# Optimization experiments

Hardware: AMD Instinct MI355X
Metric: run time of the kernel (lower is better)

## Reference

```python
import jax, jax.numpy as jnp
import numpy as np
import math

# ---- static config (matches init_kwargs) ----
MUL = 16                       # multiplicity of 0e and 1o irreps in/out
IN_DIM = 4 * MUL               # 16x0e + 16x1o -> 16 + 48 = 64 channels
DIAMETER = 7.0
RADIUS = DIAMETER / 2.0
NRB = 8                        # num_radial_basis
STEPS = (1.0, 1.0, 1.0)
N_PATHS = 5                    # 0x0->0, 1x1->0, 0x1->1, 1x0->1, 1x1->1
WEIGHT_NUMEL = N_PATHS * MUL * MUL  # 1280


def _lattice():
    axes = []
    for st in STEPS:
        s = math.floor(RADIUS / st)
        axes.append(np.arange(-s, s + 1.0) * st)
    return np.stack(np.meshgrid(*axes, indexing='ij'), axis=-1).astype(np.float32)  # [kx,ky,kz,3]


def _radial_emb(r):
    # e3nn soft_one_hot_linspace, basis='smooth_finite', cutoff=True
    values = np.linspace(0.0, RADIUS, NRB + 2)[1:-1].astype(np.float32)
    step = values[1] - values[0]
    diff = (r[..., None] - values) / step
    def u(t):  # soft unit step: exp(-1/t) for t>0 else 0
        return np.where(t > 0.0, np.exp(-1.0 / np.where(t > 0.0, t, 1.0)), 0.0)
    return (1.14136 * math.e ** 2 * u(diff + 1.0) * u(1.0 - diff)).astype(np.float32)


def _spherical_harmonics(lat):
    # normalize=True, normalization='component': Y0 = 1, Y1 = sqrt(3) * unit_vec
    n = np.linalg.norm(lat, axis=-1, keepdims=True)
    unit = np.where(n > 0, lat / np.where(n > 0, n, 1.0), 0.0)
    return np.ones(lat.shape[:-1], np.float32), (math.sqrt(3.0) * unit).astype(np.float32)


_LAT = _lattice()
_EMB = jnp.asarray(_radial_emb(np.linalg.norm(_LAT, axis=-1)))  # [kx,ky,kz,NRB]
_sh0_np, _sh1_np = _spherical_harmonics(_LAT)
_SH0, _SH1 = jnp.asarray(_sh0_np), jnp.asarray(_sh1_np)
_eps_np = np.zeros((3, 3, 3), np.float32)
for _i, _j, _k in [(0, 1, 2), (1, 2, 0), (2, 0, 1)]:
    _eps_np[_i, _j, _k] = 1.0
    _eps_np[_i, _k, _j] = -1.0
_EPS = jnp.asarray(_eps_np)


def _build_kernel(tp_weight):
    """Radial-basis matmul + CG tensor-product -> conv kernel [out,in,kx,ky,kz]."""
    kx, ky, kz = _LAT.shape[:3]
    nk = kx * ky * kz
    w = jnp.einsum('xyzb,bn->xyzn', _EMB, tp_weight) / nk
    w = w.reshape(kx, ky, kz, N_PATHS, MUL, MUL)
    w1, w2, w3, w4, w5 = [w[..., p, :, :] for p in range(N_PATHS)]
    # e3nn path weights ('component' norm, 'element' path norm): sqrt(dim_out / fan_in)
    a0 = math.sqrt(1.0 / (2 * MUL))  # -> 0e: paths 1,2 each mul1*mul2 = MUL
    a1 = math.sqrt(3.0 / (3 * MUL))  # -> 1o: paths 3,4,5
    c1 = a0                          # w3j(0,0,0) = 1
    c2 = a0 / math.sqrt(3.0)         # w3j(1,1,0) = delta/sqrt(3)
    c3 = a1 / math.sqrt(3.0)         # w3j(0,1,1) = delta/sqrt(3)
    c4 = a1 / math.sqrt(3.0)         # w3j(1,0,1) = delta/sqrt(3)
    c5 = a1 / math.sqrt(6.0)         # w3j(1,1,1) = eps/sqrt(6)
    Kss = c1 * _SH0[..., None, None] * w1                                  # [k,u,o]
    Kvs = c2 * jnp.einsum('xyzi,xyzuo->xyzuio', _SH1, w2)                  # [k,u,3,o]
    Ksv = c3 * jnp.einsum('xyzk,xyzuo->xyzuok', _SH1, w3)                  # [k,u,o,3]
    eye3 = jnp.eye(3, dtype=w.dtype)
    Kvv = (c4 * jnp.einsum('xyz,ik,xyzuo->xyzuiok', _SH0, eye3, w4)
           + c5 * jnp.einsum('ijk,xyzj,xyzuo->xyzuiok', _EPS, _SH1, w5))   # [k,u,3,o,3]
    top = jnp.concatenate([Kss, Ksv.reshape(kx, ky, kz, MUL, 3 * MUL)], axis=-1)
    bot = jnp.concatenate([Kvs.reshape(kx, ky, kz, 3 * MUL, MUL),
                           Kvv.reshape(kx, ky, kz, 3 * MUL, 3 * MUL)], axis=-1)
    K = jnp.concatenate([top, bot], axis=-2)                               # [kx,ky,kz,in,out]
    return jnp.transpose(K, (4, 3, 0, 1, 2))                               # oixyz


def setup_inputs() -> dict:
    key = jax.random.key(0)
    k1, k2, k3, k4 = jax.random.split(key, 4)
    x = jax.random.normal(k1, (2, IN_DIM, 40, 40, 40), jnp.float32)
    sc_w0 = jax.random.normal(k2, (MUL, MUL), jnp.float32)
    sc_w1 = jax.random.normal(k3, (MUL, MUL), jnp.float32)
    tp_weight = jax.random.normal(k4, (NRB, WEIGHT_NUMEL), jnp.float32)
    return {"x": x, "sc_w0": sc_w0, "sc_w1": sc_w1, "tp_weight": tp_weight}


def reference(x, sc_w0, sc_w1, tp_weight):
    B = x.shape[0]
    sp = x.shape[2:]
    inv = 1.0 / math.sqrt(MUL)  # e3nn Linear fan-in normalization
    x0 = x[:, :MUL]                                  # [B,MUL,D,H,W]
    x1 = x[:, MUL:].reshape(B, MUL, 3, *sp)          # [B,MUL,3,D,H,W]
    sc0 = jnp.einsum('uo,budhw->bodhw', sc_w0, x0) * inv
    sc1 = jnp.einsum('uo,buidhw->boidhw', sc_w1, x1) * inv
    sc = jnp.concatenate([sc0, sc1.reshape(B, 3 * MUL, *sp)], axis=1)
    K = _build_kernel(tp_weight)
    pad = [(s // 2, s // 2) for s in K.shape[2:]]
    conv = jax.lax.conv_general_dilated(
        x, K, window_strides=(1, 1, 1), padding=pad,
        dimension_numbers=('NCDHW', 'OIDHW', 'NCDHW'))
    return sc + conv
```

## Files before the change

### kernel.cpp

```cpp
#include <hip/hip_runtime.h>
#include <stdint.h>


#define NT_REAL 179
#define NT_PAD  180
#define NGRP    45

typedef short s16x8 __attribute__((ext_vector_type(8)));
typedef float f32x4 __attribute__((ext_vector_type(4)));

struct Taps {
  int n;
  short dl16[NT_PAD];
  unsigned char dz[NT_PAD], dy[NT_PAD], dx[NT_PAD];
};
constexpr Taps mk_taps() {
  Taps t{};
  t.n = 0;
  for (int a = 0; a < 7; ++a)
    for (int b = 0; b < 7; ++b)
      for (int c = 0; c < 7; ++c) {
        int d2 = (a-3)*(a-3) + (b-3)*(b-3) + (c-3)*(c-3);
        if (d2 <= 12) {
          t.dz[t.n] = (unsigned char)a; t.dy[t.n] = (unsigned char)b;
          t.dx[t.n] = (unsigned char)c;
          t.dl16[t.n] = (short)((a*14 + b)*16 + c);
          ++t.n;
        }
      }
  for (int i = t.n; i < NT_PAD; ++i) {
    t.dz[i] = 3; t.dy[i] = 3; t.dx[i] = 3; t.dl16[i] = t.dl16[0];
  }
  return t;
}
__device__ constexpr Taps TAPS = mk_taps();
static_assert(mk_taps().n == NT_REAL, "tap count");

static __device__ inline unsigned short f2bf(float f) {
  unsigned int u = __float_as_uint(f);
  unsigned int r = u + 0x7FFFu + ((u >> 16) & 1u);
  return (unsigned short)(r >> 16);
}

__device__ __forceinline__ void gl_lds16(const void* g, void* s) {
  __builtin_amdgcn_global_load_lds(
      (const __attribute__((address_space(1))) void*)g,
      (__attribute__((address_space(3))) void*)s, 16, 0, 0);
}

__global__ void build_w(const float* __restrict__ scw0, const float* __restrict__ scw1,
                        const float* __restrict__ tpw, unsigned short* __restrict__ Bwp) {
  int t = blockIdx.x;
  int tid = threadIdx.x;
  __shared__ float wsm[5][16][16];

  int dz = TAPS.dz[t], dy = TAPS.dy[t], dx = TAPS.dx[t];
  float fz = dz - 3.0f, fy = dy - 3.0f, fx = dx - 3.0f;
  float d2 = fz*fz + fy*fy + fx*fx;
  float r = sqrtf(d2);

  const float step = 3.5f / 9.0f;
  const float Cc = 1.14136f * 7.38905609893065f;
  float emb[8];
  for (int bb = 0; bb < 8; ++bb) {
    float diff = (r - step * (bb + 1)) / step;
    float t1 = diff + 1.0f, t2 = 1.0f - diff;
    float u1 = (t1 > 0.0f) ? expf(-1.0f / t1) : 0.0f;
    float u2 = (t2 > 0.0f) ? expf(-1.0f / t2) : 0.0f;
    emb[bb] = Cc * u1 * u2;
  }

  int u = tid >> 4, o = tid & 15;
  for (int p = 0; p < 5; ++p) {
    float acc = 0.0f;
    int nidx = (p * 16 + u) * 16 + o;
    for (int bb = 0; bb < 8; ++bb) acc += emb[bb] * tpw[bb * 1280 + nidx];
    wsm[p][u][o] = acc * (1.0f / 343.0f);
  }
  __syncthreads();

  float invr = (d2 > 0.0f) ? (1.7320508075688772f / r) : 0.0f;
  float sh[3] = { fz * invr, fy * invr, fx * invr };

  bool center = (dz == 3 && dy == 3 && dx == 3);
  bool padt = (t >= NT_REAL);
  const float c1 = 0.17677669529663687f;
  const float c2 = 0.10206207261596575f;
  const float c3 = 0.14433756729740643f;
  const float c4 = 0.14433756729740643f;
  const float c5 = 0.10206207261596575f;
  const float inv = 0.25f;

  for (int e = tid; e < 4096; e += 256) {
    int ich = e & 63, och = e >> 6;
    float v = 0.0f;
    if (!padt) {
      if (och < 16) {
        if (ich < 16) {
          v = c1 * wsm[0][ich][och];
          if (center) v += inv * scw0[ich * 16 + och];
        } else {
          int qq = ich - 16; int uu = qq / 3, ii = qq % 3;
          v = c2 * sh[ii] * wsm[1][uu][och];
        }
      } else {
        int qo = och - 16; int oo = qo / 3, kk = qo % 3;
        if (ich < 16) {
          v = c3 * sh[kk] * wsm[2][ich][oo];
        } else {
          int qi = ich - 16; int uu = qi / 3, ii = qi % 3;
          if (ii == kk) {
            v = c4 * wsm[3][uu][oo];
            if (center) v += inv * scw1[uu * 16 + oo];
          } else {
            int jj = 3 - ii - kk;
            float sgn = (((kk - ii + 3) % 3) == 2) ? 1.0f : -1.0f;
            v = c5 * sgn * sh[jj] * wsm[4][uu][oo];
          }
        }
      }
    }
    int chunk = ich >> 3, j = ich & 7, q = t & 3, grp = t >> 2;
    int nt = och >> 4, n = och & 15;
    size_t idx = (((((size_t)chunk * NGRP + grp) * 4 + nt) * 4 + q) * 16 + n) * 8 + j;
    Bwp[idx] = f2bf(v);
  }
}

__global__ void pad_cvt(const float* __restrict__ x, unsigned short* __restrict__ Xp) {
  __shared__ float buf[46 * 65];
  int blk = blockIdx.x;
  int yp = blk % 46; int t = blk / 46; int zp = t % 46; int b = t / 46;
  int iz = zp - 3, iy = yp - 3;
  bool rowin = ((unsigned)iz < 40u) && ((unsigned)iy < 40u);
  int tid = threadIdx.x;
  if (rowin) {
    const float* src = x + (size_t)b * 4096000 + (size_t)iz * 1600 + (size_t)iy * 40;
    for (int e = tid; e < 64 * 46; e += 256) {
      int ch = e / 46, xp = e - ch * 46;
      int ix = xp - 3;
      float v = ((unsigned)ix < 40u) ? src[(size_t)ch * 64000 + ix] : 0.0f;
      buf[xp * 65 + ch] = v;
    }
  }
  __syncthreads();
  for (int f = tid; f < 46 * 8; f += 256) {
    int xp = f >> 3, g = f & 7;
    s16x8 v = s16x8{0, 0, 0, 0, 0, 0, 0, 0};
    if (rowin) {
      #pragma unroll
      for (int j = 0; j < 8; ++j) v[j] = (short)f2bf(buf[xp * 65 + g * 8 + j]);
    }
    *reinterpret_cast<s16x8*>(Xp + ((size_t)blk * 46 + xp) * 64 + g * 8) = v;
  }
}

__global__ __launch_bounds__(512) void conv3d(
    const unsigned short* __restrict__ Xp,
    const unsigned short* __restrict__ Bwp,
    float* __restrict__ out) {
  __shared__ __align__(16) unsigned char smem[141312];
  unsigned char* XH = smem;
  unsigned char* BB = smem + 100352;

  int blk = blockIdx.x;
  int p = ((blk & 7) << 5) | (blk >> 3);
  if (p >= 250) return;
  int b = p / 125; int rem = p - b * 125;
  int tz = rem / 25, ty = (rem / 5) % 5, tx = rem % 5;

  int tid = threadIdx.x;
  int lane = tid & 63;
  int w = tid >> 6;
  int q = lane >> 4, n = lane & 15;

  const unsigned char* xg = (const unsigned char*)Xp
      + (size_t)(((b * 46 + tz * 8) * 46 + ty * 8) * 46 + tx * 8) * 128;

  int abase = w * 224 + ((n >> 3) << 4) + (n & 7);

  f32x4 acc[4][4];
  #pragma unroll
  for (int a = 0; a < 4; ++a)
    #pragma unroll
    for (int nt = 0; nt < 4; ++nt) acc[a][nt] = f32x4{0.f, 0.f, 0.f, 0.f};

  auto stageB = [&](int c, int s, unsigned char* dst) {
    const unsigned char* bg = (const unsigned char*)Bwp
        + ((size_t)c * NGRP + s * 5) * 4096;
    for (int k = w; k < 20; k += 8)
      gl_lds16(bg + (k << 10) + lane * 16, dst + (k << 10));
  };
  auto stageH = [&](int c, unsigned char* dst) {
    for (int k = w; k < 49; k += 8) {
      int sl = (k << 6) + lane;
      int hx = sl & 15; hx = hx > 13 ? 13 : hx;
      int r = sl >> 4;
      int hz = (r * 2341) >> 15;
      int hy = r - hz * 14;
      gl_lds16(xg + ((size_t)((hz * 46 + hy) * 46 + hx)) * 128 + c * 16,
               dst + (k << 10));
    }
  };

  stageB(0, 0, BB);
  stageH(0, XH);

  int t = 0;
  for (int c = 0; c < 8; ++c) {
    const unsigned char* XHc = XH + (c & 1) * 50176;
    for (int s = 0; s < 9; ++s, ++t) {
      __syncthreads();
      if (t + 1 < 72) {
        int cn = (s == 8) ? c + 1 : c;
        int sn = (s == 8) ? 0 : s + 1;
        stageB(cn, sn, BB + ((t + 1) & 1) * 20480);
      }
      if (s == 0 && c < 7) stageH(c + 1, XH + ((c + 1) & 1) * 50176);

      const unsigned char* BSc = BB + (t & 1) * 20480 + (size_t)lane * 16;
      #pragma unroll
      for (int gg = 0; gg < 5; ++gg) {
        int tb = (s * 5 + gg) << 2;
        int d0 = TAPS.dl16[tb], d1 = TAPS.dl16[tb + 1];
        int d2_ = TAPS.dl16[tb + 2], d3 = TAPS.dl16[tb + 3];
        int dl = (q == 0) ? d0 : (q == 1) ? d1 : (q == 2) ? d2_ : d3;
        const unsigned char* ab = XHc + ((size_t)(abase + dl) << 4);
        s16x8 a0 = *(const s16x8*)(ab);
        s16x8 a1 = *(const s16x8*)(ab + 512);
        s16x8 a2 = *(const s16x8*)(ab + 1024);
        s16x8 a3 = *(const s16x8*)(ab + 1536);
        const unsigned char* bp = BSc + (gg << 12);
        s16x8 b0 = *(const s16x8*)(bp);
        s16x8 b1 = *(const s16x8*)(bp + 1024);
        s16x8 b2 = *(const s16x8*)(bp + 2048);
        s16x8 b3 = *(const s16x8*)(bp + 3072);
        acc[0][0] = __builtin_amdgcn_mfma_f32_16x16x32_bf16(a0, b0, acc[0][0], 0, 0, 0);
        acc[0][1] = __builtin_amdgcn_mfma_f32_16x16x32_bf16(a0, b1, acc[0][1], 0, 0, 0);
        acc[0][2] = __builtin_amdgcn_mfma_f32_16x16x32_bf16(a0, b2, acc[0][2], 0, 0, 0);
        acc[0][3] = __builtin_amdgcn_mfma_f32_16x16x32_bf16(a0, b3, acc[0][3], 0, 0, 0);
        acc[1][0] = __builtin_amdgcn_mfma_f32_16x16x32_bf16(a1, b0, acc[1][0], 0, 0, 0);
        acc[1][1] = __builtin_amdgcn_mfma_f32_16x16x32_bf16(a1, b1, acc[1][1], 0, 0, 0);
        acc[1][2] = __builtin_amdgcn_mfma_f32_16x16x32_bf16(a1, b2, acc[1][2], 0, 0, 0);
        acc[1][3] = __builtin_amdgcn_mfma_f32_16x16x32_bf16(a1, b3, acc[1][3], 0, 0, 0);
        acc[2][0] = __builtin_amdgcn_mfma_f32_16x16x32_bf16(a2, b0, acc[2][0], 0, 0, 0);
        acc[2][1] = __builtin_amdgcn_mfma_f32_16x16x32_bf16(a2, b1, acc[2][1], 0, 0, 0);
        acc[2][2] = __builtin_amdgcn_mfma_f32_16x16x32_bf16(a2, b2, acc[2][2], 0, 0, 0);
        acc[2][3] = __builtin_amdgcn_mfma_f32_16x16x32_bf16(a2, b3, acc[2][3], 0, 0, 0);
        acc[3][0] = __builtin_amdgcn_mfma_f32_16x16x32_bf16(a3, b0, acc[3][0], 0, 0, 0);
        acc[3][1] = __builtin_amdgcn_mfma_f32_16x16x32_bf16(a3, b1, acc[3][1], 0, 0, 0);
        acc[3][2] = __builtin_amdgcn_mfma_f32_16x16x32_bf16(a3, b2, acc[3][2], 0, 0, 0);
        acc[3][3] = __builtin_amdgcn_mfma_f32_16x16x32_bf16(a3, b3, acc[3][3], 0, 0, 0);
      }
    }
  }

  #pragma unroll
  for (int nt = 0; nt < 4; ++nt) {
    size_t cb = (size_t)(b * 64 + nt * 16 + n) * 64000
              + (size_t)(tz * 8 + w) * 1600
              + (size_t)(tx * 8 + (q & 1) * 4);
    #pragma unroll
    for (int a = 0; a < 4; ++a) {
      float* dst = out + cb + (size_t)(ty * 8 + a * 2 + (q >> 1)) * 40;
      *reinterpret_cast<f32x4*>(dst) = acc[a][nt];
    }
  }
}

extern "C" void kernel_launch(void* const* d_in, const int* in_sizes, int n_in,
                              void* d_out, int out_size, void* d_ws, size_t ws_size,
                              hipStream_t stream) {
  const float* x    = (const float*)d_in[0];
  const float* scw0 = (const float*)d_in[1];
  const float* scw1 = (const float*)d_in[2];
  const float* tpw  = (const float*)d_in[3];
  float* out = (float*)d_out;

  unsigned short* Xp  = (unsigned short*)d_ws;
  unsigned short* Bwp = Xp + (size_t)2 * 46 * 46 * 46 * 64;

  build_w<<<NT_PAD, 256, 0, stream>>>(scw0, scw1, tpw, Bwp);
  pad_cvt<<<2 * 46 * 46, 256, 0, stream>>>(x, Xp);
  conv3d<<<256, 512, 0, stream>>>(Xp, Bwp, out);
}
```

Baseline: 289.1 us.

## Fuse prep kernels and double per-wave M tile in conv3d

Merges the pad/convert and weight-build kernels into one launch, with the two jobs split by block index, to remove one kernel launch. The conv3d kernel goes from 8 waves to 4 waves per block, and each wave now computes two z-slices (8 A fragments by 4 B fragments) instead of one. This doubles the reuse of each B fragment loaded from LDS per MFMA. In exchange, accumulator registers double to 128 floats per lane and there is half as much wave-level parallelism to hide LDS and global latency.

```diff
diff --git a/kernel.cpp b/kernel.cpp
--- a/kernel.cpp
+++ b/kernel.cpp
@@ -48,11 +48,41 @@
       (__attribute__((address_space(3))) void*)s, 16, 0, 0);
 }
 
-__global__ void build_w(const float* __restrict__ scw0, const float* __restrict__ scw1,
-                        const float* __restrict__ tpw, unsigned short* __restrict__ Bwp) {
-  int t = blockIdx.x;
+__global__ void prep(const float* __restrict__ x, const float* __restrict__ scw0,
+                     const float* __restrict__ scw1, const float* __restrict__ tpw,
+                     unsigned short* __restrict__ Xp, unsigned short* __restrict__ Bwp) {
+  __shared__ float buf[46 * 65];
   int tid = threadIdx.x;
-  __shared__ float wsm[5][16][16];
+
+  if (blockIdx.x < 4232) {
+    int blk = blockIdx.x;
+    int yp = blk % 46; int t = blk / 46; int zp = t % 46; int b = t / 46;
+    int iz = zp - 3, iy = yp - 3;
+    bool rowin = ((unsigned)iz < 40u) && ((unsigned)iy < 40u);
+    if (rowin) {
+      const float* src = x + (size_t)b * 4096000 + (size_t)iz * 1600 + (size_t)iy * 40;
+      for (int e = tid; e < 64 * 46; e += 256) {
+        int ch = e / 46, xp = e - ch * 46;
+        int ix = xp - 3;
+        float v = ((unsigned)ix < 40u) ? src[(size_t)ch * 64000 + ix] : 0.0f;
+        buf[xp * 65 + ch] = v;
+      }
+    }
+    __syncthreads();
+    for (int f = tid; f < 46 * 8; f += 256) {
+      int xp = f >> 3, g = f & 7;
+      s16x8 v = s16x8{0, 0, 0, 0, 0, 0, 0, 0};
+      if (rowin) {
+        #pragma unroll
+        for (int j = 0; j < 8; ++j) v[j] = (short)f2bf(buf[xp * 65 + g * 8 + j]);
+      }
+      *reinterpret_cast<s16x8*>(Xp + ((size_t)blk * 46 + xp) * 64 + g * 8) = v;
+    }
+    return;
+  }
+
+  int t = blockIdx.x - 4232;
+  float (*wsm)[16][16] = reinterpret_cast<float (*)[16][16]>(buf);
 
   int dz = TAPS.dz[t], dy = TAPS.dy[t], dx = TAPS.dx[t];
   float fz = dz - 3.0f, fy = dy - 3.0f, fx = dx - 3.0f;
@@ -127,35 +157,7 @@
   }
 }
 
-__global__ void pad_cvt(const float* __restrict__ x, unsigned short* __restrict__ Xp) {
-  __shared__ float buf[46 * 65];
-  int blk = blockIdx.x;
-  int yp = blk % 46; int t = blk / 46; int zp = t % 46; int b = t / 46;
-  int iz = zp - 3, iy = yp - 3;
-  bool rowin = ((unsigned)iz < 40u) && ((unsigned)iy < 40u);
-  int tid = threadIdx.x;
-  if (rowin) {
-    const float* src = x + (size_t)b * 4096000 + (size_t)iz * 1600 + (size_t)iy * 40;
-    for (int e = tid; e < 64 * 46; e += 256) {
-      int ch = e / 46, xp = e - ch * 46;
-      int ix = xp - 3;
-      float v = ((unsigned)ix < 40u) ? src[(size_t)ch * 64000 + ix] : 0.0f;
-      buf[xp * 65 + ch] = v;
-    }
-  }
-  __syncthreads();
-  for (int f = tid; f < 46 * 8; f += 256) {
-    int xp = f >> 3, g = f & 7;
-    s16x8 v = s16x8{0, 0, 0, 0, 0, 0, 0, 0};
-    if (rowin) {
-      #pragma unroll
-      for (int j = 0; j < 8; ++j) v[j] = (short)f2bf(buf[xp * 65 + g * 8 + j]);
-    }
-    *reinterpret_cast<s16x8*>(Xp + ((size_t)blk * 46 + xp) * 64 + g * 8) = v;
-  }
-}
-
-__global__ __launch_bounds__(512) void conv3d(
+__global__ __launch_bounds__(256) void conv3d(
     const unsigned short* __restrict__ Xp,
     const unsigned short* __restrict__ Bwp,
     float* __restrict__ out) {
@@ -177,22 +179,22 @@
   const unsigned char* xg = (const unsigned char*)Xp
       + (size_t)(((b * 46 + tz * 8) * 46 + ty * 8) * 46 + tx * 8) * 128;
 
-  int abase = w * 224 + ((n >> 3) << 4) + (n & 7);
-
-  f32x4 acc[4][4];
+  int abase = w * 448 + ((n >> 3) << 4) + (n & 7);
+
+  f32x4 acc[8][4];
   #pragma unroll
-  for (int a = 0; a < 4; ++a)
+  for (int a = 0; a < 8; ++a)
     #pragma unroll
     for (int nt = 0; nt < 4; ++nt) acc[a][nt] = f32x4{0.f, 0.f, 0.f, 0.f};
 
   auto stageB = [&](int c, int s, unsigned char* dst) {
     const unsigned char* bg = (const unsigned char*)Bwp
         + ((size_t)c * NGRP + s * 5) * 4096;
-    for (int k = w; k < 20; k += 8)
+    for (int k = w; k < 20; k += 4)
       gl_lds16(bg + (k << 10) + lane * 16, dst + (k << 10));
   };
   auto stageH = [&](int c, unsigned char* dst) {
-    for (int k = w; k < 49; k += 8) {
+    for (int k = w; k < 49; k += 4) {
       int sl = (k << 6) + lane;
       int hx = sl & 15; hx = hx > 13 ? 13 : hx;
       int r = sl >> 4;
@@ -205,6 +207,8 @@
 
   stageB(0, 0, BB);
   stageH(0, XH);
+
+  const int AOF[8] = {0, 512, 1024, 1536, 3584, 4096, 4608, 5120};
 
   int t = 0;
   for (int c = 0; c < 8; ++c) {
@@ -226,31 +230,24 @@
         int d2_ = TAPS.dl16[tb + 2], d3 = TAPS.dl16[tb + 3];
         int dl = (q == 0) ? d0 : (q == 1) ? d1 : (q == 2) ? d2_ : d3;
         const unsigned char* ab = XHc + ((size_t)(abase + dl) << 4);
-        s16x8 a0 = *(const s16x8*)(ab);
-        s16x8 a1 = *(const s16x8*)(ab + 512);
-        s16x8 a2 = *(const s16x8*)(ab + 1024);
-        s16x8 a3 = *(const s16x8*)(ab + 1536);
+
+        s16x8 afr[8];
+        #pragma unroll
+        for (int a = 0; a < 8; ++a)
+          afr[a] = *(const s16x8*)(ab + AOF[a]);
+
         const unsigned char* bp = BSc + (gg << 12);
-        s16x8 b0 = *(const s16x8*)(bp);
-        s16x8 b1 = *(const s16x8*)(bp + 1024);
-        s16x8 b2 = *(const s16x8*)(bp + 2048);
-        s16x8 b3 = *(const s16x8*)(bp + 3072);
-        acc[0][0] = __builtin_amdgcn_mfma_f32_16x16x32_bf16(a0, b0, acc[0][0], 0, 0, 0);
-        acc[0][1] = __builtin_amdgcn_mfma_f32_16x16x32_bf16(a0, b1, acc[0][1], 0, 0, 0);
-        acc[0][2] = __builtin_amdgcn_mfma_f32_16x16x32_bf16(a0, b2, acc[0][2], 0, 0, 0);
-        acc[0][3] = __builtin_amdgcn_mfma_f32_16x16x32_bf16(a0, b3, acc[0][3], 0, 0, 0);
-        acc[1][0] = __builtin_amdgcn_mfma_f32_16x16x32_bf16(a1, b0, acc[1][0], 0, 0, 0);
-        acc[1][1] = __builtin_amdgcn_mfma_f32_16x16x32_bf16(a1, b1, acc[1][1], 0, 0, 0);
-        acc[1][2] = __builtin_amdgcn_mfma_f32_16x16x32_bf16(a1, b2, acc[1][2], 0, 0, 0);
-        acc[1][3] = __builtin_amdgcn_mfma_f32_16x16x32_bf16(a1, b3, acc[1][3], 0, 0, 0);
-        acc[2][0] = __builtin_amdgcn_mfma_f32_16x16x32_bf16(a2, b0, acc[2][0], 0, 0, 0);
-        acc[2][1] = __builtin_amdgcn_mfma_f32_16x16x32_bf16(a2, b1, acc[2][1], 0, 0, 0);
-        acc[2][2] = __builtin_amdgcn_mfma_f32_16x16x32_bf16(a2, b2, acc[2][2], 0, 0, 0);
-        acc[2][3] = __builtin_amdgcn_mfma_f32_16x16x32_bf16(a2, b3, acc[2][3], 0, 0, 0);
-        acc[3][0] = __builtin_amdgcn_mfma_f32_16x16x32_bf16(a3, b0, acc[3][0], 0, 0, 0);
-        acc[3][1] = __builtin_amdgcn_mfma_f32_16x16x32_bf16(a3, b1, acc[3][1], 0, 0, 0);
-        acc[3][2] = __builtin_amdgcn_mfma_f32_16x16x32_bf16(a3, b2, acc[3][2], 0, 0, 0);
-        acc[3][3] = __builtin_amdgcn_mfma_f32_16x16x32_bf16(a3, b3, acc[3][3], 0, 0, 0);
+        s16x8 bfr[4];
+        #pragma unroll
+        for (int nt = 0; nt < 4; ++nt)
+          bfr[nt] = *(const s16x8*)(bp + (nt << 10));
+
+        #pragma unroll
+        for (int a = 0; a < 8; ++a)
+          #pragma unroll
+          for (int nt = 0; nt < 4; ++nt)
+            acc[a][nt] = __builtin_amdgcn_mfma_f32_16x16x32_bf16(
+                afr[a], bfr[nt], acc[a][nt], 0, 0, 0);
       }
     }
   }
@@ -258,11 +255,12 @@
   #pragma unroll
   for (int nt = 0; nt < 4; ++nt) {
     size_t cb = (size_t)(b * 64 + nt * 16 + n) * 64000
-              + (size_t)(tz * 8 + w) * 1600
+              + (size_t)(tz * 8 + 2 * w) * 1600
+              + (size_t)(ty * 8 + (q >> 1)) * 40
               + (size_t)(tx * 8 + (q & 1) * 4);
     #pragma unroll
-    for (int a = 0; a < 4; ++a) {
-      float* dst = out + cb + (size_t)(ty * 8 + a * 2 + (q >> 1)) * 40;
+    for (int a = 0; a < 8; ++a) {
+      float* dst = out + cb + (size_t)(a >> 2) * 1600 + (size_t)(a & 3) * 80;
       *reinterpret_cast<f32x4*>(dst) = acc[a][nt];
     }
   }
@@ -280,7 +278,6 @@
   unsigned short* Xp  = (unsigned short*)d_ws;
   unsigned short* Bwp = Xp + (size_t)2 * 46 * 46 * 46 * 64;
 
-  build_w<<<NT_PAD, 256, 0, stream>>>(scw0, scw1, tpw, Bwp);
-  pad_cvt<<<2 * 46 * 46, 256, 0, stream>>>(x, Xp);
-  conv3d<<<256, 512, 0, stream>>>(Xp, Bwp, out);
-}
+  prep<<<4232 + NT_PAD, 256, 0, stream>>>(x, scw0, scw1, tpw, Xp, Bwp);
+  conv3d<<<256, 256, 0, stream>>>(Xp, Bwp, out);
+}
```

Measured after the change: 325.9 us. 1.13x slower.

## Halve conv tiles to 4x8x8 with two blocks per CU, fuse prep kernels

Applied to the files above, without the earlier changes.

Each conv3d block now covers 4 z-planes with 256 threads instead of 8 z-planes with 512 threads. That doubles the grid to 500 blocks, and shrinking LDS to 75KB lets two blocks share a CU. The input halo is now loaded once per channel chunk, with barriers instead of double buffering, so halo loads are no longer overlapped with compute inside a block. The pad/convert and weight-build kernels are merged into one launch, with padding zeroed by a memset. Per-quad tap offsets now come from a packed 64-bit table. The smaller z extent also raises the halo overhead per output.

```diff
diff --git a/kernel.cpp b/kernel.cpp
--- a/kernel.cpp
+++ b/kernel.cpp
@@ -36,6 +36,20 @@
 __device__ constexpr Taps TAPS = mk_taps();
 static_assert(mk_taps().n == NT_REAL, "tap count");
 
+struct DL4s { unsigned long long v[NGRP]; };
+constexpr DL4s mk_dl4() {
+  DL4s d{};
+  Taps t = mk_taps();
+  for (int g = 0; g < NGRP; ++g) {
+    unsigned long long v = 0;
+    for (int q = 0; q < 4; ++q)
+      v |= (unsigned long long)(unsigned short)t.dl16[g * 4 + q] << (16 * q);
+    d.v[g] = v;
+  }
+  return d;
+}
+__device__ constexpr DL4s DL4 = mk_dl4();
+
 static __device__ inline unsigned short f2bf(float f) {
   unsigned int u = __float_as_uint(f);
   unsigned int r = u + 0x7FFFu + ((u >> 16) & 1u);
@@ -48,11 +62,37 @@
       (__attribute__((address_space(3))) void*)s, 16, 0, 0);
 }
 
-__global__ void build_w(const float* __restrict__ scw0, const float* __restrict__ scw1,
-                        const float* __restrict__ tpw, unsigned short* __restrict__ Bwp) {
-  int t = blockIdx.x;
+__global__ void prep(const float* __restrict__ x, const float* __restrict__ scw0,
+                     const float* __restrict__ scw1, const float* __restrict__ tpw,
+                     unsigned short* __restrict__ Xp, unsigned short* __restrict__ Bwp) {
+  __shared__ float buf[160 * 65];
   int tid = threadIdx.x;
-  __shared__ float wsm[5][16][16];
+
+  if (blockIdx.x < 800) {
+    int blk = blockIdx.x;
+    int ys = blk % 10; int t2 = blk / 10; int iz = t2 % 40; int b = t2 / 40;
+    int y0 = ys * 4;
+    const float* src = x + (size_t)b * 4096000 + (size_t)iz * 1600 + (size_t)y0 * 40;
+    for (int e = tid; e < 64 * 160; e += 256) {
+      int ch = e / 160, i = e - ch * 160;
+      buf[i * 65 + ch] = src[(size_t)ch * 64000 + i];
+    }
+    __syncthreads();
+    for (int f = tid; f < 160 * 8; f += 256) {
+      int i = f >> 3, g = f & 7;
+      int yy = i / 40, xx = i - yy * 40;
+      s16x8 v;
+      #pragma unroll
+      for (int j = 0; j < 8; ++j) v[j] = (short)f2bf(buf[i * 65 + g * 8 + j]);
+      size_t dst = ((size_t)((b * 46 + iz + 3) * 46 + (y0 + yy + 3)) * 46 + (xx + 3)) * 64
+                 + g * 8;
+      *reinterpret_cast<s16x8*>(Xp + dst) = v;
+    }
+    return;
+  }
+
+  int t = blockIdx.x - 800;
+  float (*wsm)[16][16] = reinterpret_cast<float (*)[16][16]>(buf);
 
   int dz = TAPS.dz[t], dy = TAPS.dy[t], dx = TAPS.dx[t];
   float fz = dz - 3.0f, fy = dy - 3.0f, fx = dx - 3.0f;
@@ -127,55 +167,26 @@
   }
 }
 
-__global__ void pad_cvt(const float* __restrict__ x, unsigned short* __restrict__ Xp) {
-  __shared__ float buf[46 * 65];
-  int blk = blockIdx.x;
-  int yp = blk % 46; int t = blk / 46; int zp = t % 46; int b = t / 46;
-  int iz = zp - 3, iy = yp - 3;
-  bool rowin = ((unsigned)iz < 40u) && ((unsigned)iy < 40u);
-  int tid = threadIdx.x;
-  if (rowin) {
-    const float* src = x + (size_t)b * 4096000 + (size_t)iz * 1600 + (size_t)iy * 40;
-    for (int e = tid; e < 64 * 46; e += 256) {
-      int ch = e / 46, xp = e - ch * 46;
-      int ix = xp - 3;
-      float v = ((unsigned)ix < 40u) ? src[(size_t)ch * 64000 + ix] : 0.0f;
-      buf[xp * 65 + ch] = v;
-    }
-  }
-  __syncthreads();
-  for (int f = tid; f < 46 * 8; f += 256) {
-    int xp = f >> 3, g = f & 7;
-    s16x8 v = s16x8{0, 0, 0, 0, 0, 0, 0, 0};
-    if (rowin) {
-      #pragma unroll
-      for (int j = 0; j < 8; ++j) v[j] = (short)f2bf(buf[xp * 65 + g * 8 + j]);
-    }
-    *reinterpret_cast<s16x8*>(Xp + ((size_t)blk * 46 + xp) * 64 + g * 8) = v;
-  }
-}
-
-__global__ __launch_bounds__(512) void conv3d(
+__global__ __launch_bounds__(256, 2) void conv3d(
     const unsigned short* __restrict__ Xp,
     const unsigned short* __restrict__ Bwp,
     float* __restrict__ out) {
-  __shared__ __align__(16) unsigned char smem[141312];
+  __shared__ __align__(16) unsigned char smem[76800];
   unsigned char* XH = smem;
-  unsigned char* BB = smem + 100352;
-
-  int blk = blockIdx.x;
-  int p = ((blk & 7) << 5) | (blk >> 3);
-  if (p >= 250) return;
-  int b = p / 125; int rem = p - b * 125;
+  unsigned char* BB = smem + 35840;
+
+  int p = blockIdx.x;
+  int b = p / 250; int rem = p - b * 250;
   int tz = rem / 25, ty = (rem / 5) % 5, tx = rem % 5;
 
   int tid = threadIdx.x;
   int lane = tid & 63;
   int w = tid >> 6;
   int q = lane >> 4, n = lane & 15;
+  int qs = q << 4;
 
   const unsigned char* xg = (const unsigned char*)Xp
-      + (size_t)(((b * 46 + tz * 8) * 46 + ty * 8) * 46 + tx * 8) * 128;
+      + (size_t)(((b * 46 + tz * 4) * 46 + ty * 8) * 46 + tx * 8) * 128;
 
   int abase = w * 224 + ((n >> 3) << 4) + (n & 7);
 
@@ -188,44 +199,39 @@
   auto stageB = [&](int c, int s, unsigned char* dst) {
     const unsigned char* bg = (const unsigned char*)Bwp
         + ((size_t)c * NGRP + s * 5) * 4096;
-    for (int k = w; k < 20; k += 8)
+    for (int k = w; k < 20; k += 4)
       gl_lds16(bg + (k << 10) + lane * 16, dst + (k << 10));
   };
-  auto stageH = [&](int c, unsigned char* dst) {
-    for (int k = w; k < 49; k += 8) {
+  auto stageH = [&](int c) {
+    for (int k = w; k < 35; k += 4) {
       int sl = (k << 6) + lane;
       int hx = sl & 15; hx = hx > 13 ? 13 : hx;
       int r = sl >> 4;
       int hz = (r * 2341) >> 15;
       int hy = r - hz * 14;
       gl_lds16(xg + ((size_t)((hz * 46 + hy) * 46 + hx)) * 128 + c * 16,
-               dst + (k << 10));
+               XH + (k << 10));
     }
   };
 
   stageB(0, 0, BB);
-  stageH(0, XH);
 
   int t = 0;
   for (int c = 0; c < 8; ++c) {
-    const unsigned char* XHc = XH + (c & 1) * 50176;
+    stageH(c);
+    __syncthreads();
     for (int s = 0; s < 9; ++s, ++t) {
-      __syncthreads();
       if (t + 1 < 72) {
         int cn = (s == 8) ? c + 1 : c;
         int sn = (s == 8) ? 0 : s + 1;
         stageB(cn, sn, BB + ((t + 1) & 1) * 20480);
       }
-      if (s == 0 && c < 7) stageH(c + 1, XH + ((c + 1) & 1) * 50176);
-
       const unsigned char* BSc = BB + (t & 1) * 20480 + (size_t)lane * 16;
       #pragma unroll
       for (int gg = 0; gg < 5; ++gg) {
-        int tb = (s * 5 + gg) << 2;
-        int d0 = TAPS.dl16[tb], d1 = TAPS.dl16[tb + 1];
-        int d2_ = TAPS.dl16[tb + 2], d3 = TAPS.dl16[tb + 3];
-        int dl = (q == 0) ? d0 : (q == 1) ? d1 : (q == 2) ? d2_ : d3;
-        const unsigned char* ab = XHc + ((size_t)(abase + dl) << 4);
+        unsigned long long dlv = DL4.v[s * 5 + gg];
+        int dl = (int)((dlv >> qs) & 0xFFFFull);
+        const unsigned char* ab = XH + ((size_t)(abase + dl) << 4);
         s16x8 a0 = *(const s16x8*)(ab);
         s16x8 a1 = *(const s16x8*)(ab + 512);
         s16x8 a2 = *(const s16x8*)(ab + 1024);
@@ -252,13 +258,14 @@
         acc[3][2] = __builtin_amdgcn_mfma_f32_16x16x32_bf16(a3, b2, acc[3][2], 0, 0, 0);
         acc[3][3] = __builtin_amdgcn_mfma_f32_16x16x32_bf16(a3, b3, acc[3][3], 0, 0, 0);
       }
+      __syncthreads();
     }
   }
 
   #pragma unroll
   for (int nt = 0; nt < 4; ++nt) {
     size_t cb = (size_t)(b * 64 + nt * 16 + n) * 64000
-              + (size_t)(tz * 8 + w) * 1600
+              + (size_t)(tz * 4 + w) * 1600
               + (size_t)(tx * 8 + (q & 1) * 4);
     #pragma unroll
     for (int a = 0; a < 4; ++a) {
@@ -280,7 +287,7 @@
   unsigned short* Xp  = (unsigned short*)d_ws;
   unsigned short* Bwp = Xp + (size_t)2 * 46 * 46 * 46 * 64;
 
-  build_w<<<NT_PAD, 256, 0, stream>>>(scw0, scw1, tpw, Bwp);
-  pad_cvt<<<2 * 46 * 46, 256, 0, stream>>>(x, Xp);
-  conv3d<<<256, 512, 0, stream>>>(Xp, Bwp, out);
-}
+  hipMemsetAsync(Xp, 0, (size_t)2 * 46 * 46 * 46 * 64 * 2, stream);
+  prep<<<800 + NT_PAD, 256, 0, stream>>>(x, scw0, scw1, tpw, Xp, Bwp);
+  conv3d<<<500, 256, 0, stream>>>(Xp, Bwp, out);
+}
```

Result: no change. 292.0 us (+1.0%).
